# Performance work log

Hardware: AMD Instinct MI355X
Metric: run time of the kernel (lower is better)

The kernel has to match this reference:

```python
import jax, jax.numpy as jnp
import numpy as np

B, L, K, D_IN, UNITS, LATENT = 4, 4096, 32, 128, 128, 64


def setup_inputs() -> dict:
    key = jax.random.key(0)
    ks = jax.random.split(key, 8)
    s = 1.0 / np.sqrt(D_IN)
    return {
        "x": jax.random.normal(ks[0], (B, L, D_IN), jnp.float32),
        "position_embedding": jax.random.normal(ks[1], (B, L, K, UNITS), jnp.float32),
        "nn_idx": jax.random.randint(ks[2], (B, L, K), 0, L, jnp.int32),
        "Wq": jax.random.normal(ks[3], (D_IN, UNITS), jnp.float32) * s,
        "Wk": jax.random.normal(ks[4], (D_IN, UNITS), jnp.float32) * s,
        "Wv": jax.random.normal(ks[5], (D_IN, UNITS), jnp.float32) * s,
        "Wa0": jax.random.normal(ks[6], (UNITS, LATENT), jnp.float32) * (1.0 / np.sqrt(UNITS)),
        "Wa1": jax.random.normal(ks[7], (LATENT, UNITS), jnp.float32) * (1.0 / np.sqrt(LATENT)),
    }


def reference(x, position_embedding, nn_idx, Wq, Wk, Wv, Wa0, Wa1):
    # projections: [B,L,units]
    query = x @ Wq
    key = x @ Wk
    value = x @ Wv

    # per-batch gather of K neighbors along the length axis -> [B,L,K,units]
    gather = jax.vmap(lambda t, idx: t[idx])
    key_n = gather(key, nn_idx)
    val_n = gather(value, nn_idx)

    # relative query-key relation: [B,L,K,units]
    qk = query[:, :, None, :] - key_n

    # position-aware attention MLP: relu(Dense) -> Dense, softmax over neighbor axis K
    attn = jax.nn.relu((qk + position_embedding) @ Wa0) @ Wa1
    attn = jax.nn.softmax(attn, axis=-2)  # per-channel softmax over K

    # weighted aggregation over neighbors -> [B,L,units]
    out = jnp.sum((val_n + position_embedding) * attn, axis=-2)
    return out
```

## Files before the change

### kernel.cpp

```cpp
#include <hip/hip_runtime.h>

#define BL 16384
#define LQ 4096

typedef unsigned int uint;
typedef __attribute__((ext_vector_type(8))) short short8;
typedef __attribute__((ext_vector_type(4))) float floatx4;

union F8 { uint u[4]; uint4 u4; short8 s; };

static __device__ __forceinline__ uint f2bf(float f) {
    uint x = __float_as_uint(f);
    x += 0x7fffu + ((x >> 16) & 1u);
    return x >> 16;
}
static __device__ __forceinline__ float bf2f(uint h) { return __uint_as_float(h << 16); }
static __device__ __forceinline__ uint pk(float lo, float hi) {
    return f2bf(lo) | (f2bf(hi) << 16);
}

static __device__ __forceinline__ uint cvtpk(float lo, float hi) {
    uint r;
    asm("v_cvt_pk_bf16_f32 %0, %1, %2" : "=v"(r) : "v"(lo), "v"(hi));
    return r;
}

__global__ __launch_bounds__(256, 4) void qkv_mfma(
    const float* __restrict__ x, const float* __restrict__ Wq,
    const float* __restrict__ Wk, const float* __restrict__ Wv,
    float* __restrict__ qkvb)
{
    __shared__ uint4 wfh[4][8][64];
    __shared__ uint4 wfl[4][8][64];
    const int tid  = threadIdx.x;
    const int lane = tid & 63;
    const int w    = tid >> 6;
    const int q    = lane >> 4;
    const int c    = lane & 15;
    const int proj = blockIdx.y;
    const float* W = (proj == 0) ? Wq : (proj == 1) ? Wk : Wv;
    float* outb = qkvb + (size_t)proj * BL * 128;

    for (int e = tid; e < 32 * 64; e += 256) {
        const int f = e >> 6, ln = e & 63;
        const int ks = f >> 3, Nt = f & 7;
        const int lq = ln >> 4, lc = ln & 15;
        const float* wp = W + (ks * 32 + lq * 8) * 128 + Nt * 16 + lc;
        F8 hi, lo;
        #pragma unroll
        for (int j = 0; j < 4; ++j) {
            const float a = wp[(2 * j) * 128], b = wp[(2 * j + 1) * 128];
            const uint ha = f2bf(a), hb = f2bf(b);
            hi.u[j] = ha | (hb << 16);
            lo.u[j] = pk(a - bf2f(ha), b - bf2f(hb));
        }
        wfh[ks][Nt][ln] = hi.u4;
        wfl[ks][Nt][ln] = lo.u4;
    }
    __syncthreads();

    floatx4 acc[8];
    #pragma unroll
    for (int i = 0; i < 8; ++i) acc[i] = {0.f, 0.f, 0.f, 0.f};

    const int arow = blockIdx.x * 64 + w * 16 + c;
    #pragma unroll
    for (int ks = 0; ks < 4; ++ks) {
        const float* xp = x + arow * 128 + ks * 32 + q * 8;
        const float4 xa = ((const float4*)xp)[0];
        const float4 xb = ((const float4*)xp)[1];
        const float xv[8] = {xa.x, xa.y, xa.z, xa.w, xb.x, xb.y, xb.z, xb.w};
        F8 xh, xl;
        #pragma unroll
        for (int j = 0; j < 4; ++j) {
            const uint ha = f2bf(xv[2 * j]), hb = f2bf(xv[2 * j + 1]);
            xh.u[j] = ha | (hb << 16);
            xl.u[j] = pk(xv[2 * j] - bf2f(ha), xv[2 * j + 1] - bf2f(hb));
        }
        #pragma unroll
        for (int Nt = 0; Nt < 8; ++Nt) {
            F8 wh, wl;
            wh.u4 = wfh[ks][Nt][lane];
            wl.u4 = wfl[ks][Nt][lane];
            acc[Nt] = __builtin_amdgcn_mfma_f32_16x16x32_bf16(xh.s, wh.s, acc[Nt], 0, 0, 0);
            acc[Nt] = __builtin_amdgcn_mfma_f32_16x16x32_bf16(xh.s, wl.s, acc[Nt], 0, 0, 0);
            acc[Nt] = __builtin_amdgcn_mfma_f32_16x16x32_bf16(xl.s, wh.s, acc[Nt], 0, 0, 0);
        }
    }
    const int orow = blockIdx.x * 64 + w * 16 + q * 4;
    #pragma unroll
    for (int Nt = 0; Nt < 8; ++Nt)
        #pragma unroll
        for (int r = 0; r < 4; ++r)
            outb[(orow + r) * 128 + Nt * 16 + c] = acc[Nt][r];
}

__global__ __launch_bounds__(256, 4) void attn_mfma(
    const float* __restrict__ pos, const int* __restrict__ nn_idx,
    const float* __restrict__ qb, const float* __restrict__ kb,
    const float* __restrict__ vb, const float* __restrict__ Wa0,
    const float* __restrict__ Wa1, float* __restrict__ out)
{
    __shared__ uint4 wa0f[16][64];
    __shared__ uint4 wa1f[16][64];
    const int tid  = threadIdx.x;
    const int lane = tid & 63;
    const int w    = tid >> 6;
    const int q    = lane >> 4;
    const int c    = lane & 15;

    for (int e = tid; e < 16 * 64; e += 256) {
        const int f = e >> 6, ln = e & 63;
        const int Mt = f >> 2, ks = f & 3;
        const int lq = ln >> 4, lc = ln & 15;
        const float* wp = Wa0 + (ks * 32 + lq * 8) * 64 + Mt * 16 + lc;
        F8 v;
        #pragma unroll
        for (int j = 0; j < 4; ++j) v.u[j] = cvtpk(wp[(2 * j) * 64], wp[(2 * j + 1) * 64]);
        wa0f[f][ln] = v.u4;
    }
    for (int e = tid; e < 16 * 64; e += 256) {
        const int f = e >> 6, ln = e & 63;
        const int ks = f >> 3, Nt = f & 7;
        const int lq = ln >> 4, lc = ln & 15;
        const float* wp = Wa1 + (ks * 32 + lq * 8) * 128 + Nt * 16 + lc;
        F8 v;
        #pragma unroll
        for (int j = 0; j < 4; ++j) v.u[j] = cvtpk(wp[(2 * j) * 128], wp[(2 * j + 1) * 128]);
        wa1f[f][ln] = v.u4;
    }
    __syncthreads();

    const int p     = blockIdx.x * 4 + w;
    const int bbase = (p >> 12) << 12;

    const int idx0 = nn_idx[p * 32 + c];
    const int idx1 = nn_idx[p * 32 + 16 + c];
    const int r0   = (bbase + idx0) * 128;
    const int r1   = (bbase + idx1) * 128;
    const int pr0  = (p * 32 + c) * 128;
    const int pr1  = pr0 + 16 * 128;

    floatx4 acc1[4][2];
    #pragma unroll
    for (int i = 0; i < 4; ++i) { acc1[i][0] = {0.f,0.f,0.f,0.f}; acc1[i][1] = {0.f,0.f,0.f,0.f}; }

    #pragma unroll
    for (int ks = 0; ks < 4; ++ks) {
        const int u0 = ks * 32 + q * 8;
        const float4 qa = *(const float4*)(qb + p * 128 + u0);
        const float4 qc = *(const float4*)(qb + p * 128 + u0 + 4);
        F8 bfrag[2];
        #pragma unroll
        for (int Nt = 0; Nt < 2; ++Nt) {
            const int kr = (Nt == 0 ? r0 : r1) + u0;
            const int pr = (Nt == 0 ? pr0 : pr1) + u0;
            const float4 ka = *(const float4*)(kb + kr);
            const float4 kc = *(const float4*)(kb + kr + 4);
            const float4 pa = *(const float4*)(pos + pr);
            const float4 pc = *(const float4*)(pos + pr + 4);
            const float t0 = qa.x - ka.x + pa.x, t1 = qa.y - ka.y + pa.y;
            const float t2 = qa.z - ka.z + pa.z, t3 = qa.w - ka.w + pa.w;
            const float t4 = qc.x - kc.x + pc.x, t5 = qc.y - kc.y + pc.y;
            const float t6 = qc.z - kc.z + pc.z, t7 = qc.w - kc.w + pc.w;
            bfrag[Nt].u[0] = cvtpk(t0, t1); bfrag[Nt].u[1] = cvtpk(t2, t3);
            bfrag[Nt].u[2] = cvtpk(t4, t5); bfrag[Nt].u[3] = cvtpk(t6, t7);
        }
        #pragma unroll
        for (int Mt = 0; Mt < 4; ++Mt) {
            F8 a1; a1.u4 = wa0f[Mt * 4 + ks][lane];
            acc1[Mt][0] = __builtin_amdgcn_mfma_f32_16x16x32_bf16(a1.s, bfrag[0].s, acc1[Mt][0], 0, 0, 0);
            acc1[Mt][1] = __builtin_amdgcn_mfma_f32_16x16x32_bf16(a1.s, bfrag[1].s, acc1[Mt][1], 0, 0, 0);
        }
    }

    F8 a2[2][2];
    #pragma unroll
    for (int Mt2 = 0; Mt2 < 2; ++Mt2) {
        #pragma unroll
        for (int ks = 0; ks < 2; ++ks) {
            float vv[8];
            #pragma unroll
            for (int t = 0; t < 8; ++t) {
                const int sl = c + 16 * ((q & 1) * 2 + (t >> 2));
                const float vA = __shfl(acc1[2 * ks + 0][Mt2][t & 3], sl, 64);
                const float vB = __shfl(acc1[2 * ks + 1][Mt2][t & 3], sl, 64);
                vv[t] = fmaxf((q < 2) ? vA : vB, 0.f);
            }
            #pragma unroll
            for (int j = 0; j < 4; ++j) a2[Mt2][ks].u[j] = cvtpk(vv[2 * j], vv[2 * j + 1]);
        }
    }

    int vrow[2][4], prow[2][4];
    #pragma unroll
    for (int Mt2 = 0; Mt2 < 2; ++Mt2)
        #pragma unroll
        for (int r = 0; r < 4; ++r) {
            const int knb  = Mt2 * 16 + q * 4 + r;
            const int sidx = __shfl(Mt2 == 0 ? idx0 : idx1, q * 4 + r, 64);
            vrow[Mt2][r] = (bbase + sidx) * 128;
            prow[Mt2][r] = (p * 32 + knb) * 128;
        }

    #pragma unroll
    for (int Nt2 = 0; Nt2 < 8; ++Nt2) {
        F8 b0, b1;
        b0.u4 = wa1f[Nt2][lane];
        b1.u4 = wa1f[8 + Nt2][lane];
        floatx4 a2c[2];
        a2c[0] = {0.f,0.f,0.f,0.f}; a2c[1] = {0.f,0.f,0.f,0.f};
        #pragma unroll
        for (int Mt2 = 0; Mt2 < 2; ++Mt2) {
            a2c[Mt2] = __builtin_amdgcn_mfma_f32_16x16x32_bf16(a2[Mt2][0].s, b0.s, a2c[Mt2], 0, 0, 0);
            a2c[Mt2] = __builtin_amdgcn_mfma_f32_16x16x32_bf16(a2[Mt2][1].s, b1.s, a2c[Mt2], 0, 0, 0);
        }
        const int cg = Nt2 * 16 + c;
        float se = 0.f, ov = 0.f;
        #pragma unroll
        for (int Mt2 = 0; Mt2 < 2; ++Mt2)
            #pragma unroll
            for (int r = 0; r < 4; ++r) {
                const float e  = __expf(a2c[Mt2][r]);
                const float vp = vb[vrow[Mt2][r] + cg] + pos[prow[Mt2][r] + cg];
                se += e;
                ov = fmaf(e, vp, ov);
            }
        se += __shfl_xor(se, 16, 64); ov += __shfl_xor(ov, 16, 64);
        se += __shfl_xor(se, 32, 64); ov += __shfl_xor(ov, 32, 64);
        if (q == 0) out[p * 128 + cg] = ov / se;
    }
}

extern "C" void kernel_launch(void* const* d_in, const int* in_sizes, int n_in,
                              void* d_out, int out_size, void* d_ws, size_t ws_size,
                              hipStream_t stream) {
    const float* x    = (const float*)d_in[0];
    const float* pos  = (const float*)d_in[1];
    const int*   nidx = (const int*)  d_in[2];
    const float* Wq   = (const float*)d_in[3];
    const float* Wk   = (const float*)d_in[4];
    const float* Wv   = (const float*)d_in[5];
    const float* Wa0  = (const float*)d_in[6];
    const float* Wa1  = (const float*)d_in[7];
    float* outp = (float*)d_out;

    float* qkvb = (float*)d_ws;
    const float* qbp = qkvb;
    const float* kbp = qkvb + (size_t)BL * 128;
    const float* vbp = qkvb + (size_t)2 * BL * 128;

    qkv_mfma<<<dim3(BL / 64, 3), 256, 0, stream>>>(x, Wq, Wk, Wv, qkvb);
    attn_mfma<<<BL / 4, 256, 0, stream>>>(pos, nidx, qbp, kbp, vbp, Wa0, Wa1, outp);
}
```

Baseline: 477.7 us.

## Stage per-point position-embedding tile into LDS via async global_load_lds

Each wave copies its point's 32x128 position-embedding tile into swizzled shared memory with direct global-to-LDS loads. Both the first MLP input and the final value aggregation then read it from LDS instead of global memory. This removes the second pass over the largest input tensor. The cost is 64KB of LDS per block, which forces launch bounds down to one block per CU and reduces latency hiding for the neighbor gathers.

Result: slower. 510.9 us (+7.0%).

```diff
diff --git a/kernel.cpp b/kernel.cpp
--- a/kernel.cpp
+++ b/kernel.cpp
@@ -23,6 +23,19 @@
     uint r;
     asm("v_cvt_pk_bf16_f32 %0, %1, %2" : "=v"(r) : "v"(lo), "v"(hi));
     return r;
+}
+
+static __device__ __forceinline__ void stage16(const void* g, void* l) {
+    __builtin_amdgcn_global_load_lds(
+        (const __attribute__((address_space(1))) uint*)g,
+        (__attribute__((address_space(3))) uint*)l, 16, 0, 0);
+}
+
+static __device__ __forceinline__ float4 rdpos4(const float* pb, int k, int ub) {
+    return *(const float4*)((const char*)pb + ((k * 512 + ub) ^ ((k & 7) << 4)));
+}
+static __device__ __forceinline__ float rdpos1(const float* pb, int k, int col) {
+    return *(const float*)((const char*)pb + ((k * 512 + col * 4) ^ ((k & 7) << 4)));
 }
 
 __global__ __launch_bounds__(256, 4) void qkv_mfma(
@@ -95,7 +108,7 @@
             outb[(orow + r) * 128 + Nt * 16 + c] = acc[Nt][r];
 }
 
-__global__ __launch_bounds__(256, 4) void attn_mfma(
+__global__ __launch_bounds__(256, 1) void attn_mfma(
     const float* __restrict__ pos, const int* __restrict__ nn_idx,
     const float* __restrict__ qb, const float* __restrict__ kb,
     const float* __restrict__ vb, const float* __restrict__ Wa0,
@@ -103,11 +116,31 @@
 {
     __shared__ uint4 wa0f[16][64];
     __shared__ uint4 wa1f[16][64];
+    __shared__ float posb[4][4096];
     const int tid  = threadIdx.x;
     const int lane = tid & 63;
     const int w    = tid >> 6;
     const int q    = lane >> 4;
     const int c    = lane & 15;
+
+    const int p     = blockIdx.x * 4 + w;
+    const int bbase = (p >> 12) << 12;
+
+    {
+        const char* ptile = (const char*)(pos + (size_t)p * 4096);
+        char* lbase = (char*)&posb[w][0];
+        #pragma unroll
+        for (int i = 0; i < 16; ++i) {
+            const int row = i * 2 + (lane >> 5);
+            const int off = (i * 1024 + lane * 16) ^ ((row & 7) << 4);
+            stage16(ptile + off, lbase + i * 1024);
+        }
+    }
+
+    const int idx0 = nn_idx[p * 32 + c];
+    const int idx1 = nn_idx[p * 32 + 16 + c];
+    const int r0   = (bbase + idx0) * 128;
+    const int r1   = (bbase + idx1) * 128;
 
     for (int e = tid; e < 16 * 64; e += 256) {
         const int f = e >> 6, ln = e & 63;
@@ -131,15 +164,7 @@
     }
     __syncthreads();
 
-    const int p     = blockIdx.x * 4 + w;
-    const int bbase = (p >> 12) << 12;
-
-    const int idx0 = nn_idx[p * 32 + c];
-    const int idx1 = nn_idx[p * 32 + 16 + c];
-    const int r0   = (bbase + idx0) * 128;
-    const int r1   = (bbase + idx1) * 128;
-    const int pr0  = (p * 32 + c) * 128;
-    const int pr1  = pr0 + 16 * 128;
+    const float* pb = &posb[w][0];
 
     floatx4 acc1[4][2];
     #pragma unroll
@@ -153,12 +178,12 @@
         F8 bfrag[2];
         #pragma unroll
         for (int Nt = 0; Nt < 2; ++Nt) {
-            const int kr = (Nt == 0 ? r0 : r1) + u0;
-            const int pr = (Nt == 0 ? pr0 : pr1) + u0;
+            const int kr   = (Nt == 0 ? r0 : r1) + u0;
+            const int krow = (Nt == 0 ? c : c + 16);
             const float4 ka = *(const float4*)(kb + kr);
             const float4 kc = *(const float4*)(kb + kr + 4);
-            const float4 pa = *(const float4*)(pos + pr);
-            const float4 pc = *(const float4*)(pos + pr + 4);
+            const float4 pa = rdpos4(pb, krow, ks * 128 + q * 32);
+            const float4 pc = rdpos4(pb, krow, ks * 128 + q * 32 + 16);
             const float t0 = qa.x - ka.x + pa.x, t1 = qa.y - ka.y + pa.y;
             const float t2 = qa.z - ka.z + pa.z, t3 = qa.w - ka.w + pa.w;
             const float t4 = qc.x - kc.x + pc.x, t5 = qc.y - kc.y + pc.y;
@@ -192,15 +217,13 @@
         }
     }
 
-    int vrow[2][4], prow[2][4];
+    int vrow[2][4];
     #pragma unroll
     for (int Mt2 = 0; Mt2 < 2; ++Mt2)
         #pragma unroll
         for (int r = 0; r < 4; ++r) {
-            const int knb  = Mt2 * 16 + q * 4 + r;
             const int sidx = __shfl(Mt2 == 0 ? idx0 : idx1, q * 4 + r, 64);
             vrow[Mt2][r] = (bbase + sidx) * 128;
-            prow[Mt2][r] = (p * 32 + knb) * 128;
         }
 
     #pragma unroll
@@ -221,8 +244,9 @@
         for (int Mt2 = 0; Mt2 < 2; ++Mt2)
             #pragma unroll
             for (int r = 0; r < 4; ++r) {
+                const int knb = Mt2 * 16 + q * 4 + r;
                 const float e  = __expf(a2c[Mt2][r]);
-                const float vp = vb[vrow[Mt2][r] + cg] + pos[prow[Mt2][r] + cg];
+                const float vp = vb[vrow[Mt2][r] + cg] + rdpos1(pb, knb, cg);
                 se += e;
                 ov = fmaf(e, vp, ov);
             }
```
